# Performance work log

Measured on AMD Instinct MI355X. Metric: run time of the kernel, lower is better.

The kernel has to match this reference:

```python
import jax, jax.numpy as jnp
import numpy as np

N = 50000
E = 800000
IN_C, HID_C, OUT_C = 128, 128, 64


def setup_inputs() -> dict:
    key = jax.random.key(0)
    k_x, k_e, k_w1, k_w2 = jax.random.split(key, 4)
    x = jax.random.normal(k_x, (N, IN_C), dtype=jnp.float32)
    edge_index = jax.random.randint(k_e, (2, E), 0, N, dtype=jnp.int64)
    # glorot-ish init scale
    W1 = jax.random.normal(k_w1, (IN_C, HID_C), dtype=jnp.float32) * (1.0 / np.sqrt(IN_C))
    b1 = jnp.zeros((HID_C,), dtype=jnp.float32)
    W2 = jax.random.normal(k_w2, (HID_C, OUT_C), dtype=jnp.float32) * (1.0 / np.sqrt(HID_C))
    b2 = jnp.zeros((OUT_C,), dtype=jnp.float32)
    return {"x": x, "edge_index": edge_index, "W1": W1, "b1": b1, "W2": W2, "b2": b2}


def _gcn_norm(edge_index, num_nodes):
    # PyG gcn_norm with add_self_loops=True: deg over destination (col), sym norm
    loops = jnp.arange(num_nodes, dtype=edge_index.dtype)
    src = jnp.concatenate([edge_index[0], loops])
    dst = jnp.concatenate([edge_index[1], loops])
    deg = jax.ops.segment_sum(jnp.ones_like(dst, dtype=jnp.float32), dst, num_segments=num_nodes)
    dinv = jnp.where(deg > 0, jax.lax.rsqrt(deg), 0.0)
    norm = dinv[src] * dinv[dst]  # [E+N]
    return src, dst, norm


def _gcn_conv(x, src, dst, norm, W, b, num_nodes):
    h = x @ W                              # [N, out]
    msg = h[src] * norm[:, None]           # [E+N, out] gather + scale
    agg = jax.ops.segment_sum(msg, dst, num_segments=num_nodes)  # scatter-add
    return agg + b


def reference(x, edge_index, W1, b1, W2, b2):
    num_nodes = x.shape[0]
    src, dst, norm = _gcn_norm(edge_index, num_nodes)
    h = _gcn_conv(x, src, dst, norm, W1, b1, num_nodes)
    h = jax.nn.relu(h)
    out = _gcn_conv(h, src, dst, norm, W2, b2, num_nodes)
    return out
```

## Files before the change

kernel.cpp:

```cpp
#include <hip/hip_runtime.h>
#include <hip/hip_bf16.h>


#define IN_C 128
#define HID_C 128
#define OUT_C 64
#define BKT_SH 8
#define BKT_NODES 256
#define CHUNK 4096
#define CAPB 6144
#define OVF_CAP 65536

typedef float f32x4 __attribute__((ext_vector_type(4)));
typedef short bf16x8 __attribute__((ext_vector_type(8)));

__device__ inline unsigned short f2bf_rtn(float f) {
  unsigned u = __float_as_uint(f);
  unsigned r = u + 0x7fffu + ((u >> 16) & 1u);
  return (unsigned short)(r >> 16);
}
__device__ inline unsigned pack_bf2(float a, float b) {
  return (unsigned)f2bf_rtn(a) | ((unsigned)f2bf_rtn(b) << 16);
}

__global__ __launch_bounds__(256) void wt_zero_kernel(
    const float* __restrict__ W1, const float* __restrict__ W2,
    short* __restrict__ w1t, short* __restrict__ w2t,
    int* __restrict__ zbase, int zints) {
  int i = blockIdx.x * 256 + threadIdx.x;
  if (i < zints) zbase[i] = 0;
  if (i < IN_C * HID_C) {
    int n = i >> 7, k = i & 127;
    w1t[i] = (short)f2bf_rtn(W1[k * HID_C + n]);
  }
  if (i < HID_C * OUT_C) {
    int n = i >> 7, k = i & 127;
    w2t[i] = (short)f2bf_rtn(W2[k * OUT_C + n]);
  }
}

__global__ __launch_bounds__(256) void p1_gemm1_kernel(
    const int* __restrict__ ei, unsigned* __restrict__ pairs,
    int* __restrict__ bcnt, uint2* __restrict__ ovf, int* __restrict__ ovf_cnt,
    int* __restrict__ ovfb, int E, int K, int P1B,
    const float* __restrict__ X, const short* __restrict__ Wt,
    unsigned short* __restrict__ H, int ntiles) {
  int t = threadIdx.x;
  if ((int)blockIdx.x < P1B) {
    __shared__ unsigned buf[CHUNK];
    __shared__ int hist[256];
    __shared__ int lofs[256];
    __shared__ int cur[256];
    __shared__ int gbase[256];
    __shared__ int ws4[4];
    int base_e = blockIdx.x * CHUNK;
    int cnt_e = E - base_e;
    if (cnt_e > CHUNK) cnt_e = CHUNK;

    hist[t] = 0;
    __syncthreads();

    for (int i = t; i < cnt_e; i += 256)
      atomicAdd(&hist[ei[E + base_e + i] >> BKT_SH], 1);
    __syncthreads();

    int v = hist[t];
    int lane = t & 63, wid = t >> 6;
    int inc = v;
    #pragma unroll
    for (int off = 1; off < 64; off <<= 1) {
      int u = __shfl_up(inc, off, 64);
      if (lane >= off) inc += u;
    }
    if (lane == 63) ws4[wid] = inc;
    __syncthreads();
    if (t == 0) {
      int a = ws4[0], b = ws4[1], c = ws4[2];
      ws4[0] = 0; ws4[1] = a; ws4[2] = a + b; ws4[3] = a + b + c;
    }
    __syncthreads();
    int excl = ws4[wid] + inc - v;
    lofs[t] = excl;
    cur[t] = excl;
    if (t < K && v > 0) gbase[t] = atomicAdd(&bcnt[t], v);
    __syncthreads();

    for (int i = t; i < cnt_e; i += 256) {
      int src = ei[base_e + i];
      int dst = ei[E + base_e + i];
      int b = dst >> BKT_SH;
      int pos = atomicAdd(&cur[b], 1);
      buf[pos] = (unsigned)src | ((unsigned)(dst & (BKT_NODES - 1)) << 16) |
                 ((unsigned)b << 24);
    }
    __syncthreads();

    for (int i = t; i < cnt_e; i += 256) {
      unsigned w = buf[i];
      int b = w >> 24;
      int g = gbase[b] + (i - lofs[b]);
      if (g < CAPB) {
        pairs[(size_t)b * CAPB + g] = w;
      } else {
        int oi = atomicAdd(ovf_cnt, 1);
        if (oi < OVF_CAP) {
          unsigned dst = (unsigned)(b << BKT_SH) | ((w >> 16) & 0xFFu);
          ovf[oi] = make_uint2(w & 0xFFFFu, dst);
          atomicAdd(&ovfb[b], 1);
        }
      }
    }
  } else {
    int lane = t & 63;
    int tile = ((int)blockIdx.x - P1B) * 4 + (t >> 6);
    if (tile >= ntiles) return;
    constexpr int NT = HID_C / 16;

    int arow = tile * 16 + (lane & 15);
    int kch = (lane >> 4) * 8;

    bf16x8 afrag[4];
    const float4* Xf = (const float4*)X;
    #pragma unroll
    for (int kt = 0; kt < 4; ++kt) {
      float4 f0 = Xf[(size_t)arow * 32 + (kt * 32 + kch) / 4];
      float4 f1 = Xf[(size_t)arow * 32 + (kt * 32 + kch) / 4 + 1];
      bf16x8 a;
      a[0] = (short)f2bf_rtn(f0.x); a[1] = (short)f2bf_rtn(f0.y);
      a[2] = (short)f2bf_rtn(f0.z); a[3] = (short)f2bf_rtn(f0.w);
      a[4] = (short)f2bf_rtn(f1.x); a[5] = (short)f2bf_rtn(f1.y);
      a[6] = (short)f2bf_rtn(f1.z); a[7] = (short)f2bf_rtn(f1.w);
      afrag[kt] = a;
    }

    const bf16x8* W8 = (const bf16x8*)Wt;
    f32x4 zero = {0.f, 0.f, 0.f, 0.f};
    f32x4 acc[NT];
    #pragma unroll
    for (int ct = 0; ct < NT; ++ct) acc[ct] = zero;

    #pragma unroll
    for (int ct = 0; ct < NT; ++ct) {
      int bcol = ct * 16 + (lane & 15);
      #pragma unroll
      for (int kt = 0; kt < 4; ++kt) {
        bf16x8 b = W8[bcol * 16 + (kt * 32 + kch) / 8];
        acc[ct] = __builtin_amdgcn_mfma_f32_16x16x32_bf16(afrag[kt], b, acc[ct], 0, 0, 0);
      }
    }

    int r0 = tile * 16 + (lane >> 4) * 4;
    #pragma unroll
    for (int ct = 0; ct < NT; ++ct) {
      #pragma unroll
      for (int j = 0; j < 4; ++j)
        H[(size_t)(r0 + j) * HID_C + ct * 16 + (lane & 15)] = f2bf_rtn(acc[ct][j]);
    }
  }
}

__global__ __launch_bounds__(256) void phase2_csr_kernel(
    const unsigned* __restrict__ pairs, const int* __restrict__ bcnt,
    const int* __restrict__ ovfb, const uint2* __restrict__ ovf,
    const int* __restrict__ ovf_cnt, int* __restrict__ rowstart,
    float* __restrict__ dinv, unsigned short* __restrict__ csr, int N, int K) {
  int b = blockIdx.x;
  int t = threadIdx.x;
  __shared__ int hist[BKT_NODES];
  __shared__ int cur[BKT_NODES];
  __shared__ int sbase[256];
  __shared__ int ws4[4];
  int lane = t & 63, wid = t >> 6;

  int cb = 0;
  if (t < K) {
    int c = bcnt[t];
    cb = (c < CAPB ? c : CAPB) + ovfb[t];
  }
  {
    int inc = cb;
    #pragma unroll
    for (int off = 1; off < 64; off <<= 1) {
      int u = __shfl_up(inc, off, 64);
      if (lane >= off) inc += u;
    }
    if (lane == 63) ws4[wid] = inc;
    __syncthreads();
    if (t == 0) {
      int a = ws4[0], bb = ws4[1], c = ws4[2];
      ws4[0] = 0; ws4[1] = a; ws4[2] = a + bb; ws4[3] = a + bb + c;
    }
    __syncthreads();
    int excl = ws4[wid] + inc - cb;
    sbase[t] = excl;
    if (b == K - 1 && t == K - 1) rowstart[N] = excl + cb;
  }
  __syncthreads();
  int base = sbase[b];

  hist[t] = 0;
  __syncthreads();

  int cnt = bcnt[b];
  if (cnt > CAPB) cnt = CAPB;
  const unsigned* reg = pairs + (size_t)b * CAPB;

  for (int i = t; i < cnt; i += 256)
    atomicAdd(&hist[(reg[i] >> 16) & 0xFFu], 1);
  int oc = *ovf_cnt;
  if (oc > OVF_CAP) oc = OVF_CAP;
  for (int i = t; i < oc; i += 256) {
    uint2 p = ovf[i];
    if ((int)(p.y >> BKT_SH) == b) atomicAdd(&hist[p.y & (BKT_NODES - 1)], 1);
  }
  __syncthreads();

  int v = hist[t];
  int inc = v;
  #pragma unroll
  for (int off = 1; off < 64; off <<= 1) {
    int u = __shfl_up(inc, off, 64);
    if (lane >= off) inc += u;
  }
  __syncthreads();
  if (lane == 63) ws4[wid] = inc;
  __syncthreads();
  if (t == 0) {
    int a = ws4[0], bb = ws4[1], c = ws4[2];
    ws4[0] = 0; ws4[1] = a; ws4[2] = a + bb; ws4[3] = a + bb + c;
  }
  __syncthreads();
  int excl = ws4[wid] + inc - v;

  int node = b * BKT_NODES + t;
  if (node < N) {
    rowstart[node] = base + excl;
    dinv[node] = rsqrtf((float)(v + 1));
  }
  cur[t] = base + excl;
  __syncthreads();

  for (int i = t; i < cnt; i += 256) {
    unsigned w = reg[i];
    int pos = atomicAdd(&cur[(w >> 16) & 0xFFu], 1);
    csr[pos] = (unsigned short)(w & 0xffffu);
  }
  for (int i = t; i < oc; i += 256) {
    uint2 p = ovf[i];
    if ((int)(p.y >> BKT_SH) == b) {
      int pos = atomicAdd(&cur[p.y & (BKT_NODES - 1)], 1);
      csr[pos] = (unsigned short)p.x;
    }
  }
}

__global__ __launch_bounds__(256) void agg1_gemm2_kernel(
    const unsigned short* __restrict__ Hs, const int* __restrict__ rowstart,
    const unsigned short* __restrict__ csr, const float* __restrict__ dinv,
    const float* __restrict__ b1, const short* __restrict__ w2t,
    unsigned short* __restrict__ H2, int n) {
  __shared__ unsigned x2s[16][64];
  int t = threadIdx.x;
  int row = t >> 4;
  int lane16 = t & 15;
  int node = blockIdx.x * 16 + row;

  float acc[8];
  #pragma unroll
  for (int j = 0; j < 8; ++j) acc[j] = 0.f;

  if (node < n) {
    const uint4* H4 = reinterpret_cast<const uint4*>(Hs);
    int s = rowstart[node];
    int e = rowstart[node + 1];
    float dnode = dinv[node];

    {
      uint4 v = H4[(size_t)node * 16 + lane16];
      acc[0] = __uint_as_float(v.x << 16) * dnode;
      acc[1] = __uint_as_float(v.x & 0xffff0000u) * dnode;
      acc[2] = __uint_as_float(v.y << 16) * dnode;
      acc[3] = __uint_as_float(v.y & 0xffff0000u) * dnode;
      acc[4] = __uint_as_float(v.z << 16) * dnode;
      acc[5] = __uint_as_float(v.z & 0xffff0000u) * dnode;
      acc[6] = __uint_as_float(v.w << 16) * dnode;
      acc[7] = __uint_as_float(v.w & 0xffff0000u) * dnode;
    }

    int p = s;
    for (; p + 1 < e; p += 2) {
      int s0 = csr[p];
      int s1 = csr[p + 1];
      uint4 v0 = H4[(size_t)s0 * 16 + lane16];
      uint4 v1 = H4[(size_t)s1 * 16 + lane16];
      float d0 = dinv[s0], d1 = dinv[s1];
      acc[0] = fmaf(__uint_as_float(v0.x << 16), d0, acc[0]);
      acc[1] = fmaf(__uint_as_float(v0.x & 0xffff0000u), d0, acc[1]);
      acc[2] = fmaf(__uint_as_float(v0.y << 16), d0, acc[2]);
      acc[3] = fmaf(__uint_as_float(v0.y & 0xffff0000u), d0, acc[3]);
      acc[4] = fmaf(__uint_as_float(v0.z << 16), d0, acc[4]);
      acc[5] = fmaf(__uint_as_float(v0.z & 0xffff0000u), d0, acc[5]);
      acc[6] = fmaf(__uint_as_float(v0.w << 16), d0, acc[6]);
      acc[7] = fmaf(__uint_as_float(v0.w & 0xffff0000u), d0, acc[7]);
      acc[0] = fmaf(__uint_as_float(v1.x << 16), d1, acc[0]);
      acc[1] = fmaf(__uint_as_float(v1.x & 0xffff0000u), d1, acc[1]);
      acc[2] = fmaf(__uint_as_float(v1.y << 16), d1, acc[2]);
      acc[3] = fmaf(__uint_as_float(v1.y & 0xffff0000u), d1, acc[3]);
      acc[4] = fmaf(__uint_as_float(v1.z << 16), d1, acc[4]);
      acc[5] = fmaf(__uint_as_float(v1.z & 0xffff0000u), d1, acc[5]);
      acc[6] = fmaf(__uint_as_float(v1.w << 16), d1, acc[6]);
      acc[7] = fmaf(__uint_as_float(v1.w & 0xffff0000u), d1, acc[7]);
    }
    if (p < e) {
      int s0 = csr[p];
      uint4 v0 = H4[(size_t)s0 * 16 + lane16];
      float d0 = dinv[s0];
      acc[0] = fmaf(__uint_as_float(v0.x << 16), d0, acc[0]);
      acc[1] = fmaf(__uint_as_float(v0.x & 0xffff0000u), d0, acc[1]);
      acc[2] = fmaf(__uint_as_float(v0.y << 16), d0, acc[2]);
      acc[3] = fmaf(__uint_as_float(v0.y & 0xffff0000u), d0, acc[3]);
      acc[4] = fmaf(__uint_as_float(v0.z << 16), d0, acc[4]);
      acc[5] = fmaf(__uint_as_float(v0.z & 0xffff0000u), d0, acc[5]);
      acc[6] = fmaf(__uint_as_float(v0.w << 16), d0, acc[6]);
      acc[7] = fmaf(__uint_as_float(v0.w & 0xffff0000u), d0, acc[7]);
    }

    const float4* b4 = reinterpret_cast<const float4*>(b1);
    float4 bv0 = b4[lane16 * 2];
    float4 bv1 = b4[lane16 * 2 + 1];
    acc[0] = fmaxf(fmaf(acc[0], dnode, bv0.x), 0.f);
    acc[1] = fmaxf(fmaf(acc[1], dnode, bv0.y), 0.f);
    acc[2] = fmaxf(fmaf(acc[2], dnode, bv0.z), 0.f);
    acc[3] = fmaxf(fmaf(acc[3], dnode, bv0.w), 0.f);
    acc[4] = fmaxf(fmaf(acc[4], dnode, bv1.x), 0.f);
    acc[5] = fmaxf(fmaf(acc[5], dnode, bv1.y), 0.f);
    acc[6] = fmaxf(fmaf(acc[6], dnode, bv1.z), 0.f);
    acc[7] = fmaxf(fmaf(acc[7], dnode, bv1.w), 0.f);
  }

  x2s[row][lane16 * 4 + 0] = pack_bf2(acc[0], acc[1]);
  x2s[row][lane16 * 4 + 1] = pack_bf2(acc[2], acc[3]);
  x2s[row][lane16 * 4 + 2] = pack_bf2(acc[4], acc[5]);
  x2s[row][lane16 * 4 + 3] = pack_bf2(acc[6], acc[7]);
  __syncthreads();

  int lane = t & 63;
  int w = t >> 6;
  int kch = (lane >> 4) * 8;

  const bf16x8* W8 = (const bf16x8*)w2t;
  f32x4 oacc = {0.f, 0.f, 0.f, 0.f};
  int bcol = w * 16 + (lane & 15);
  #pragma unroll
  for (int kt = 0; kt < 4; ++kt) {
    bf16x8 a = *reinterpret_cast<const bf16x8*>(&x2s[lane & 15][kt * 16 + kch / 2]);
    bf16x8 b = W8[bcol * 16 + (kt * 32 + kch) / 8];
    oacc = __builtin_amdgcn_mfma_f32_16x16x32_bf16(a, b, oacc, 0, 0, 0);
  }

  int r0 = (lane >> 4) * 4;
  #pragma unroll
  for (int j = 0; j < 4; ++j) {
    int g = blockIdx.x * 16 + r0 + j;
    if (g < n)
      H2[(size_t)g * OUT_C + w * 16 + (lane & 15)] = f2bf_rtn(oacc[j] * dinv[g]);
  }
}

__global__ __launch_bounds__(256) void agg2_kernel(
    const unsigned short* __restrict__ Hs, const int* __restrict__ rowstart,
    const unsigned short* __restrict__ csr, const float* __restrict__ dinv,
    const float* __restrict__ bias, float* __restrict__ out, int n) {
  constexpr int TPN = OUT_C / 8;
  constexpr int NPB = 256 / TPN;
  int lane = threadIdx.x % TPN;
  int node = blockIdx.x * NPB + threadIdx.x / TPN;
  if (node >= n) return;

  const uint4* H4 = reinterpret_cast<const uint4*>(Hs);
  int s = rowstart[node];
  int e = rowstart[node + 1];

  float acc[8];
  {
    uint4 v = H4[(size_t)node * TPN + lane];
    acc[0] = __uint_as_float(v.x << 16);
    acc[1] = __uint_as_float(v.x & 0xffff0000u);
    acc[2] = __uint_as_float(v.y << 16);
    acc[3] = __uint_as_float(v.y & 0xffff0000u);
    acc[4] = __uint_as_float(v.z << 16);
    acc[5] = __uint_as_float(v.z & 0xffff0000u);
    acc[6] = __uint_as_float(v.w << 16);
    acc[7] = __uint_as_float(v.w & 0xffff0000u);
  }

  int p = s;
  for (; p + 1 < e; p += 2) {
    int s0 = csr[p];
    int s1 = csr[p + 1];
    uint4 v0 = H4[(size_t)s0 * TPN + lane];
    uint4 v1 = H4[(size_t)s1 * TPN + lane];
    acc[0] += __uint_as_float(v0.x << 16);
    acc[1] += __uint_as_float(v0.x & 0xffff0000u);
    acc[2] += __uint_as_float(v0.y << 16);
    acc[3] += __uint_as_float(v0.y & 0xffff0000u);
    acc[4] += __uint_as_float(v0.z << 16);
    acc[5] += __uint_as_float(v0.z & 0xffff0000u);
    acc[6] += __uint_as_float(v0.w << 16);
    acc[7] += __uint_as_float(v0.w & 0xffff0000u);
    acc[0] += __uint_as_float(v1.x << 16);
    acc[1] += __uint_as_float(v1.x & 0xffff0000u);
    acc[2] += __uint_as_float(v1.y << 16);
    acc[3] += __uint_as_float(v1.y & 0xffff0000u);
    acc[4] += __uint_as_float(v1.z << 16);
    acc[5] += __uint_as_float(v1.z & 0xffff0000u);
    acc[6] += __uint_as_float(v1.w << 16);
    acc[7] += __uint_as_float(v1.w & 0xffff0000u);
  }
  if (p < e) {
    int s0 = csr[p];
    uint4 v0 = H4[(size_t)s0 * TPN + lane];
    acc[0] += __uint_as_float(v0.x << 16);
    acc[1] += __uint_as_float(v0.x & 0xffff0000u);
    acc[2] += __uint_as_float(v0.y << 16);
    acc[3] += __uint_as_float(v0.y & 0xffff0000u);
    acc[4] += __uint_as_float(v0.z << 16);
    acc[5] += __uint_as_float(v0.z & 0xffff0000u);
    acc[6] += __uint_as_float(v0.w << 16);
    acc[7] += __uint_as_float(v0.w & 0xffff0000u);
  }

  float dnode = dinv[node];
  float4 b0 = reinterpret_cast<const float4*>(bias)[lane * 2];
  float4 b1 = reinterpret_cast<const float4*>(bias)[lane * 2 + 1];
  float4* o4 = reinterpret_cast<float4*>(out) + (size_t)node * (OUT_C / 4);
  o4[lane * 2] = make_float4(fmaf(acc[0], dnode, b0.x), fmaf(acc[1], dnode, b0.y),
                             fmaf(acc[2], dnode, b0.z), fmaf(acc[3], dnode, b0.w));
  o4[lane * 2 + 1] = make_float4(fmaf(acc[4], dnode, b1.x), fmaf(acc[5], dnode, b1.y),
                                 fmaf(acc[6], dnode, b1.z), fmaf(acc[7], dnode, b1.w));
}

extern "C" void kernel_launch(void* const* d_in, const int* in_sizes, int n_in,
                              void* d_out, int out_size, void* d_ws, size_t ws_size,
                              hipStream_t stream) {
  const float* x  = (const float*)d_in[0];
  const int*   ei = (const int*)d_in[1];
  const float* W1 = (const float*)d_in[2];
  const float* b1 = (const float*)d_in[3];
  const float* W2 = (const float*)d_in[4];
  const float* b2 = (const float*)d_in[5];
  float* out = (float*)d_out;

  const int N = in_sizes[0] / IN_C;
  const int E = in_sizes[1] / 2;
  const int K = (N + BKT_NODES - 1) >> BKT_SH;
  const int NTILES = (N + 15) / 16;
  const int P1B = (E + CHUNK - 1) / CHUNK;
  const int GB1 = (NTILES + 3) / 4;

  char* ws = (char*)d_ws;
  size_t off = 0;
  auto alloc = [&](size_t bytes) -> void* {
    void* p = ws + off;
    off += (bytes + 255) & ~(size_t)255;
    return p;
  };
  int* bcnt    = (int*)alloc((size_t)K * 4);
  int* ovf_cnt = (int*)alloc(4);
  int* ovfb    = (int*)alloc((size_t)K * 4);
  size_t zero_bytes = off;
  const int zints = (int)(zero_bytes / 4);

  int*   rowstart    = (int*)  alloc((size_t)(N + 1) * 4);
  float* dinv        = (float*)alloc((size_t)N * 4);
  unsigned* pairs    = (unsigned*)alloc((size_t)K * CAPB * 4);
  uint2* ovf         = (uint2*)alloc((size_t)OVF_CAP * 8);
  unsigned short* csr = (unsigned short*)alloc((size_t)E * 2);
  unsigned short* hs  = (unsigned short*)alloc((size_t)N * HID_C * 2);
  unsigned short* hs2 = (unsigned short*)alloc((size_t)N * OUT_C * 2);
  short* w1t         = (short*)alloc((size_t)IN_C * HID_C * 2);
  short* w2t         = (short*)alloc((size_t)HID_C * OUT_C * 2);

  int wt_threads = zints > IN_C * HID_C ? zints : IN_C * HID_C;
  wt_zero_kernel<<<(wt_threads + 255) / 256, 256, 0, stream>>>(
      W1, W2, w1t, w2t, (int*)ws, zints);

  p1_gemm1_kernel<<<P1B + GB1, 256, 0, stream>>>(
      ei, pairs, bcnt, ovf, ovf_cnt, ovfb, E, K, P1B, x, w1t, hs, NTILES);

  phase2_csr_kernel<<<K, 256, 0, stream>>>(
      pairs, bcnt, ovfb, ovf, ovf_cnt, rowstart, dinv, csr, N, K);

  agg1_gemm2_kernel<<<NTILES, 256, 0, stream>>>(
      hs, rowstart, csr, dinv, b1, w2t, hs2, N);

  agg2_kernel<<<(N + 31) / 32, 256, 0, stream>>>(
      hs2, rowstart, csr, dinv, b2, out, N);
}
```

Baseline: 102.9 us.

## Use one wavefront per node with edge-parallel slots in aggregation kernels

Both aggregation kernels now assign a full 64-lane wavefront to each destination node. The lanes are split into feature columns and edge slots, so several neighbor rows are gathered concurrently, and partial sums are then combined with cross-lane shuffles. The first kernel grows to 1024-thread blocks, and only the first four waves run the MFMA GEMM. The aim is more memory-level parallelism per node for the average degree of about 16 neighbors, at the cost of shuffle reductions, idle lanes on low-degree nodes and much larger blocks.

```diff
diff --git a/kernel.cpp b/kernel.cpp
--- a/kernel.cpp
+++ b/kernel.cpp
@@ -254,29 +254,32 @@
   }
 }
 
-__global__ __launch_bounds__(256) void agg1_gemm2_kernel(
+__global__ __launch_bounds__(1024) void agg1_gemm2_kernel(
     const unsigned short* __restrict__ Hs, const int* __restrict__ rowstart,
     const unsigned short* __restrict__ csr, const float* __restrict__ dinv,
     const float* __restrict__ b1, const short* __restrict__ w2t,
     unsigned short* __restrict__ H2, int n) {
   __shared__ unsigned x2s[16][64];
   int t = threadIdx.x;
-  int row = t >> 4;
-  int lane16 = t & 15;
-  int node = blockIdx.x * 16 + row;
+  int wave = t >> 6;
+  int lane = t & 63;
+  int c = lane & 15;
+  int slot = lane >> 4;
+  int node = blockIdx.x * 16 + wave;
 
   float acc[8];
   #pragma unroll
   for (int j = 0; j < 8; ++j) acc[j] = 0.f;
+  float dnode = 0.f;
 
   if (node < n) {
     const uint4* H4 = reinterpret_cast<const uint4*>(Hs);
     int s = rowstart[node];
     int e = rowstart[node + 1];
-    float dnode = dinv[node];
-
-    {
-      uint4 v = H4[(size_t)node * 16 + lane16];
+    dnode = dinv[node];
+
+    if (slot == 0) {
+      uint4 v = H4[(size_t)node * 16 + c];
       acc[0] = __uint_as_float(v.x << 16) * dnode;
       acc[1] = __uint_as_float(v.x & 0xffff0000u) * dnode;
       acc[2] = __uint_as_float(v.y << 16) * dnode;
@@ -287,83 +290,72 @@
       acc[7] = __uint_as_float(v.w & 0xffff0000u) * dnode;
     }
 
-    int p = s;
-    for (; p + 1 < e; p += 2) {
-      int s0 = csr[p];
-      int s1 = csr[p + 1];
-      uint4 v0 = H4[(size_t)s0 * 16 + lane16];
-      uint4 v1 = H4[(size_t)s1 * 16 + lane16];
-      float d0 = dinv[s0], d1 = dinv[s1];
-      acc[0] = fmaf(__uint_as_float(v0.x << 16), d0, acc[0]);
-      acc[1] = fmaf(__uint_as_float(v0.x & 0xffff0000u), d0, acc[1]);
-      acc[2] = fmaf(__uint_as_float(v0.y << 16), d0, acc[2]);
-      acc[3] = fmaf(__uint_as_float(v0.y & 0xffff0000u), d0, acc[3]);
-      acc[4] = fmaf(__uint_as_float(v0.z << 16), d0, acc[4]);
-      acc[5] = fmaf(__uint_as_float(v0.z & 0xffff0000u), d0, acc[5]);
-      acc[6] = fmaf(__uint_as_float(v0.w << 16), d0, acc[6]);
-      acc[7] = fmaf(__uint_as_float(v0.w & 0xffff0000u), d0, acc[7]);
-      acc[0] = fmaf(__uint_as_float(v1.x << 16), d1, acc[0]);
-      acc[1] = fmaf(__uint_as_float(v1.x & 0xffff0000u), d1, acc[1]);
-      acc[2] = fmaf(__uint_as_float(v1.y << 16), d1, acc[2]);
-      acc[3] = fmaf(__uint_as_float(v1.y & 0xffff0000u), d1, acc[3]);
-      acc[4] = fmaf(__uint_as_float(v1.z << 16), d1, acc[4]);
-      acc[5] = fmaf(__uint_as_float(v1.z & 0xffff0000u), d1, acc[5]);
-      acc[6] = fmaf(__uint_as_float(v1.w << 16), d1, acc[6]);
-      acc[7] = fmaf(__uint_as_float(v1.w & 0xffff0000u), d1, acc[7]);
-    }
-    if (p < e) {
-      int s0 = csr[p];
-      uint4 v0 = H4[(size_t)s0 * 16 + lane16];
-      float d0 = dinv[s0];
-      acc[0] = fmaf(__uint_as_float(v0.x << 16), d0, acc[0]);
-      acc[1] = fmaf(__uint_as_float(v0.x & 0xffff0000u), d0, acc[1]);
-      acc[2] = fmaf(__uint_as_float(v0.y << 16), d0, acc[2]);
-      acc[3] = fmaf(__uint_as_float(v0.y & 0xffff0000u), d0, acc[3]);
-      acc[4] = fmaf(__uint_as_float(v0.z << 16), d0, acc[4]);
-      acc[5] = fmaf(__uint_as_float(v0.z & 0xffff0000u), d0, acc[5]);
-      acc[6] = fmaf(__uint_as_float(v0.w << 16), d0, acc[6]);
-      acc[7] = fmaf(__uint_as_float(v0.w & 0xffff0000u), d0, acc[7]);
-    }
-
+    for (int p0 = s; p0 < e; p0 += 4) {
+      int p = p0 + slot;
+      if (p < e) {
+        int s0 = csr[p];
+        float d0 = dinv[s0];
+        uint4 v = H4[(size_t)s0 * 16 + c];
+        acc[0] = fmaf(__uint_as_float(v.x << 16), d0, acc[0]);
+        acc[1] = fmaf(__uint_as_float(v.x & 0xffff0000u), d0, acc[1]);
+        acc[2] = fmaf(__uint_as_float(v.y << 16), d0, acc[2]);
+        acc[3] = fmaf(__uint_as_float(v.y & 0xffff0000u), d0, acc[3]);
+        acc[4] = fmaf(__uint_as_float(v.z << 16), d0, acc[4]);
+        acc[5] = fmaf(__uint_as_float(v.z & 0xffff0000u), d0, acc[5]);
+        acc[6] = fmaf(__uint_as_float(v.w << 16), d0, acc[6]);
+        acc[7] = fmaf(__uint_as_float(v.w & 0xffff0000u), d0, acc[7]);
+      }
+    }
+  }
+
+  #pragma unroll
+  for (int j = 0; j < 8; ++j) {
+    acc[j] += __shfl_xor(acc[j], 16, 64);
+    acc[j] += __shfl_xor(acc[j], 32, 64);
+  }
+
+  if (slot == 0) {
     const float4* b4 = reinterpret_cast<const float4*>(b1);
-    float4 bv0 = b4[lane16 * 2];
-    float4 bv1 = b4[lane16 * 2 + 1];
-    acc[0] = fmaxf(fmaf(acc[0], dnode, bv0.x), 0.f);
-    acc[1] = fmaxf(fmaf(acc[1], dnode, bv0.y), 0.f);
-    acc[2] = fmaxf(fmaf(acc[2], dnode, bv0.z), 0.f);
-    acc[3] = fmaxf(fmaf(acc[3], dnode, bv0.w), 0.f);
-    acc[4] = fmaxf(fmaf(acc[4], dnode, bv1.x), 0.f);
-    acc[5] = fmaxf(fmaf(acc[5], dnode, bv1.y), 0.f);
-    acc[6] = fmaxf(fmaf(acc[6], dnode, bv1.z), 0.f);
-    acc[7] = fmaxf(fmaf(acc[7], dnode, bv1.w), 0.f);
-  }
-
-  x2s[row][lane16 * 4 + 0] = pack_bf2(acc[0], acc[1]);
-  x2s[row][lane16 * 4 + 1] = pack_bf2(acc[2], acc[3]);
-  x2s[row][lane16 * 4 + 2] = pack_bf2(acc[4], acc[5]);
-  x2s[row][lane16 * 4 + 3] = pack_bf2(acc[6], acc[7]);
-  __syncthreads();
-
-  int lane = t & 63;
-  int w = t >> 6;
-  int kch = (lane >> 4) * 8;
-
-  const bf16x8* W8 = (const bf16x8*)w2t;
-  f32x4 oacc = {0.f, 0.f, 0.f, 0.f};
-  int bcol = w * 16 + (lane & 15);
-  #pragma unroll
-  for (int kt = 0; kt < 4; ++kt) {
-    bf16x8 a = *reinterpret_cast<const bf16x8*>(&x2s[lane & 15][kt * 16 + kch / 2]);
-    bf16x8 b = W8[bcol * 16 + (kt * 32 + kch) / 8];
-    oacc = __builtin_amdgcn_mfma_f32_16x16x32_bf16(a, b, oacc, 0, 0, 0);
-  }
-
-  int r0 = (lane >> 4) * 4;
-  #pragma unroll
-  for (int j = 0; j < 4; ++j) {
-    int g = blockIdx.x * 16 + r0 + j;
-    if (g < n)
-      H2[(size_t)g * OUT_C + w * 16 + (lane & 15)] = f2bf_rtn(oacc[j] * dinv[g]);
+    float4 bv0 = b4[c * 2];
+    float4 bv1 = b4[c * 2 + 1];
+    float r[8];
+    r[0] = fmaxf(fmaf(acc[0], dnode, bv0.x), 0.f);
+    r[1] = fmaxf(fmaf(acc[1], dnode, bv0.y), 0.f);
+    r[2] = fmaxf(fmaf(acc[2], dnode, bv0.z), 0.f);
+    r[3] = fmaxf(fmaf(acc[3], dnode, bv0.w), 0.f);
+    r[4] = fmaxf(fmaf(acc[4], dnode, bv1.x), 0.f);
+    r[5] = fmaxf(fmaf(acc[5], dnode, bv1.y), 0.f);
+    r[6] = fmaxf(fmaf(acc[6], dnode, bv1.z), 0.f);
+    r[7] = fmaxf(fmaf(acc[7], dnode, bv1.w), 0.f);
+    x2s[wave][c * 4 + 0] = pack_bf2(r[0], r[1]);
+    x2s[wave][c * 4 + 1] = pack_bf2(r[2], r[3]);
+    x2s[wave][c * 4 + 2] = pack_bf2(r[4], r[5]);
+    x2s[wave][c * 4 + 3] = pack_bf2(r[6], r[7]);
+  }
+  __syncthreads();
+
+  if (t < 256) {
+    int w = t >> 6;
+    int l = t & 63;
+    int kch = (l >> 4) * 8;
+
+    const bf16x8* W8 = (const bf16x8*)w2t;
+    f32x4 oacc = {0.f, 0.f, 0.f, 0.f};
+    int bcol = w * 16 + (l & 15);
+    #pragma unroll
+    for (int kt = 0; kt < 4; ++kt) {
+      bf16x8 a = *reinterpret_cast<const bf16x8*>(&x2s[l & 15][kt * 16 + kch / 2]);
+      bf16x8 b = W8[bcol * 16 + (kt * 32 + kch) / 8];
+      oacc = __builtin_amdgcn_mfma_f32_16x16x32_bf16(a, b, oacc, 0, 0, 0);
+    }
+
+    int r0 = (l >> 4) * 4;
+    #pragma unroll
+    for (int j = 0; j < 4; ++j) {
+      int g = blockIdx.x * 16 + r0 + j;
+      if (g < n)
+        H2[(size_t)g * OUT_C + w * 16 + (l & 15)] = f2bf_rtn(oacc[j] * dinv[g]);
+    }
   }
 }
 
@@ -371,10 +363,12 @@
     const unsigned short* __restrict__ Hs, const int* __restrict__ rowstart,
     const unsigned short* __restrict__ csr, const float* __restrict__ dinv,
     const float* __restrict__ bias, float* __restrict__ out, int n) {
-  constexpr int TPN = OUT_C / 8;
-  constexpr int NPB = 256 / TPN;
-  int lane = threadIdx.x % TPN;
-  int node = blockIdx.x * NPB + threadIdx.x / TPN;
+  int t = threadIdx.x;
+  int wave = t >> 6;
+  int lane = t & 63;
+  int c = lane & 7;
+  int slot = lane >> 3;
+  int node = blockIdx.x * 4 + wave;
   if (node >= n) return;
 
   const uint4* H4 = reinterpret_cast<const uint4*>(Hs);
@@ -382,8 +376,11 @@
   int e = rowstart[node + 1];
 
   float acc[8];
-  {
-    uint4 v = H4[(size_t)node * TPN + lane];
+  #pragma unroll
+  for (int j = 0; j < 8; ++j) acc[j] = 0.f;
+
+  if (slot == 0) {
+    uint4 v = H4[(size_t)node * 8 + c];
     acc[0] = __uint_as_float(v.x << 16);
     acc[1] = __uint_as_float(v.x & 0xffff0000u);
     acc[2] = __uint_as_float(v.y << 16);
@@ -394,50 +391,39 @@
     acc[7] = __uint_as_float(v.w & 0xffff0000u);
   }
 
-  int p = s;
-  for (; p + 1 < e; p += 2) {
-    int s0 = csr[p];
-    int s1 = csr[p + 1];
-    uint4 v0 = H4[(size_t)s0 * TPN + lane];
-    uint4 v1 = H4[(size_t)s1 * TPN + lane];
-    acc[0] += __uint_as_float(v0.x << 16);
-    acc[1] += __uint_as_float(v0.x & 0xffff0000u);
-    acc[2] += __uint_as_float(v0.y << 16);
-    acc[3] += __uint_as_float(v0.y & 0xffff0000u);
-    acc[4] += __uint_as_float(v0.z << 16);
-    acc[5] += __uint_as_float(v0.z & 0xffff0000u);
-    acc[6] += __uint_as_float(v0.w << 16);
-    acc[7] += __uint_as_float(v0.w & 0xffff0000u);
-    acc[0] += __uint_as_float(v1.x << 16);
-    acc[1] += __uint_as_float(v1.x & 0xffff0000u);
-    acc[2] += __uint_as_float(v1.y << 16);
-    acc[3] += __uint_as_float(v1.y & 0xffff0000u);
-    acc[4] += __uint_as_float(v1.z << 16);
-    acc[5] += __uint_as_float(v1.z & 0xffff0000u);
-    acc[6] += __uint_as_float(v1.w << 16);
-    acc[7] += __uint_as_float(v1.w & 0xffff0000u);
-  }
-  if (p < e) {
-    int s0 = csr[p];
-    uint4 v0 = H4[(size_t)s0 * TPN + lane];
-    acc[0] += __uint_as_float(v0.x << 16);
-    acc[1] += __uint_as_float(v0.x & 0xffff0000u);
-    acc[2] += __uint_as_float(v0.y << 16);
-    acc[3] += __uint_as_float(v0.y & 0xffff0000u);
-    acc[4] += __uint_as_float(v0.z << 16);
-    acc[5] += __uint_as_float(v0.z & 0xffff0000u);
-    acc[6] += __uint_as_float(v0.w << 16);
-    acc[7] += __uint_as_float(v0.w & 0xffff0000u);
-  }
-
-  float dnode = dinv[node];
-  float4 b0 = reinterpret_cast<const float4*>(bias)[lane * 2];
-  float4 b1 = reinterpret_cast<const float4*>(bias)[lane * 2 + 1];
-  float4* o4 = reinterpret_cast<float4*>(out) + (size_t)node * (OUT_C / 4);
-  o4[lane * 2] = make_float4(fmaf(acc[0], dnode, b0.x), fmaf(acc[1], dnode, b0.y),
-                             fmaf(acc[2], dnode, b0.z), fmaf(acc[3], dnode, b0.w));
-  o4[lane * 2 + 1] = make_float4(fmaf(acc[4], dnode, b1.x), fmaf(acc[5], dnode, b1.y),
-                                 fmaf(acc[6], dnode, b1.z), fmaf(acc[7], dnode, b1.w));
+  for (int p0 = s; p0 < e; p0 += 8) {
+    int p = p0 + slot;
+    if (p < e) {
+      int s0 = csr[p];
+      uint4 v = H4[(size_t)s0 * 8 + c];
+      acc[0] += __uint_as_float(v.x << 16);
+      acc[1] += __uint_as_float(v.x & 0xffff0000u);
+      acc[2] += __uint_as_float(v.y << 16);
+      acc[3] += __uint_as_float(v.y & 0xffff0000u);
+      acc[4] += __uint_as_float(v.z << 16);
+      acc[5] += __uint_as_float(v.z & 0xffff0000u);
+      acc[6] += __uint_as_float(v.w << 16);
+      acc[7] += __uint_as_float(v.w & 0xffff0000u);
+    }
+  }
+
+  #pragma unroll
+  for (int j = 0; j < 8; ++j) {
+    acc[j] += __shfl_xor(acc[j], 8, 64);
+    acc[j] += __shfl_xor(acc[j], 16, 64);
+    acc[j] += __shfl_xor(acc[j], 32, 64);
+  }
+
+  if (slot == 0) {
+    float dnode = dinv[node];
+    float4 b0 = reinterpret_cast<const float4*>(bias)[c * 2];
+    float4 b1 = reinterpret_cast<const float4*>(bias)[c * 2 + 1];
+    float4* o4 = reinterpret_cast<float4*>(out) + (size_t)node * (OUT_C / 4);
+    o4[c * 2] = make_float4(fmaf(acc[0], dnode, b0.x), fmaf(acc[1], dnode, b0.y),
+                            fmaf(acc[2], dnode, b0.z), fmaf(acc[3], dnode, b0.w));
+    o4[c * 2 + 1] = make_float4(fmaf(acc[4], dnode, b1.x), fmaf(acc[5], dnode, b1.y),
+                                fmaf(acc[6], dnode, b1.z), fmaf(acc[7], dnode, b1.w));
+  }
 }
 
 extern "C" void kernel_launch(void* const* d_in, const int* in_sizes, int n_in,
@@ -491,9 +477,9 @@
   phase2_csr_kernel<<<K, 256, 0, stream>>>(
       pairs, bcnt, ovfb, ovf, ovf_cnt, rowstart, dinv, csr, N, K);
 
-  agg1_gemm2_kernel<<<NTILES, 256, 0, stream>>>(
+  agg1_gemm2_kernel<<<NTILES, 1024, 0, stream>>>(
       hs, rowstart, csr, dinv, b1, w2t, hs2, N);
 
-  agg2_kernel<<<(N + 31) / 32, 256, 0, stream>>>(
+  agg2_kernel<<<(N + 3) / 4, 256, 0, stream>>>(
       hs2, rowstart, csr, dinv, b2, out, N);
 }
```

Result: slower. 126.5 us (+22.9%).
